# Kernel optimization log

Measured on AMD Instinct MI355X. Metric: run time of the kernel, lower is better.

The kernel has to match this reference:

```python
import jax, jax.numpy as jnp
import numpy as np
from jax import lax

L, B, N, D = 6, 4, 2048, 512
H, DH = 8, 64
ID = H * DH           # 512
M = 266               # int(64*log(64)) random features
INNER = 2 * D         # conformer expansion
K = 31                # depthwise kernel
PAD = (15, 15)        # calc_same_padding(31)
EPS_LN = 1e-5


def setup_inputs() -> dict:
    key = jax.random.key(0)
    ks = jax.random.split(key, 12)
    s = 0.02
    return {
        "x": jax.random.normal(ks[0], (B, N, D), jnp.float32),
        "ln1_g": jnp.ones((L, D), jnp.float32),
        "ln1_b": jnp.zeros((L, D), jnp.float32),
        "wq": jax.random.normal(ks[1], (L, ID, D), jnp.float32) * s,
        "bq": jnp.zeros((L, ID), jnp.float32),
        "wk": jax.random.normal(ks[2], (L, ID, D), jnp.float32) * s,
        "bk": jnp.zeros((L, ID), jnp.float32),
        "wv": jax.random.normal(ks[3], (L, ID, D), jnp.float32) * s,
        "bv": jnp.zeros((L, ID), jnp.float32),
        "wo": jax.random.normal(ks[4], (L, ID, D), jnp.float32) * s,
        "bo": jnp.zeros((L, D), jnp.float32),
        # FAVOR+ random projection buffer (gaussian orthogonal ~ iid gaussian rows)
        "proj": jax.random.normal(ks[5], (L, M, DH), jnp.float32),
        "ln2_g": jnp.ones((L, D), jnp.float32),
        "ln2_b": jnp.zeros((L, D), jnp.float32),
        "pw1_w": jax.random.normal(ks[6], (L, 2 * INNER, D), jnp.float32) * s,
        "pw1_b": jnp.zeros((L, 2 * INNER), jnp.float32),
        "dw_w": jax.random.normal(ks[7], (L, INNER, K), jnp.float32) * s,
        "dw_b": jnp.zeros((L, INNER), jnp.float32),
        "pw2_w": jax.random.normal(ks[8], (L, D, INNER), jnp.float32) * s,
        "pw2_b": jnp.zeros((L, D), jnp.float32),
    }


def layer_norm(x, g, b):
    mu = jnp.mean(x, axis=-1, keepdims=True)
    var = jnp.mean((x - mu) ** 2, axis=-1, keepdims=True)
    return (x - mu) * lax.rsqrt(var + EPS_LN) * g + b


def softmax_kernel(data, proj, is_query, eps=1e-4):
    # data: [b,h,n,dh], proj: [m,dh]
    dn = DH ** -0.25
    ratio = M ** -0.5
    data_dash = jnp.einsum('bhnd,md->bhnm', dn * data, proj)
    diag = jnp.sum(data * data, axis=-1, keepdims=True) * 0.5 * dn * dn  # [b,h,n,1]
    if is_query:
        mx = jnp.max(data_dash, axis=-1, keepdims=True)
        return ratio * (jnp.exp(data_dash - diag - mx) + eps)
    else:
        return ratio * jnp.exp(data_dash - diag + eps)


def favor_attention(q, k, v, proj):
    qp = softmax_kernel(q, proj, True)   # [b,h,n,m]
    kp = softmax_kernel(k, proj, False)  # [b,h,n,m]
    k_cumsum = jnp.sum(kp, axis=-2)      # [b,h,m]
    d_inv = 1.0 / (jnp.einsum('bhnm,bhm->bhn', qp, k_cumsum) + 1e-8)
    context = jnp.einsum('bhnm,bhne->bhme', kp, v)          # [b,h,m,dh]
    out = jnp.einsum('bhme,bhnm,bhn->bhne', context, qp, d_inv)
    return out


def pcmer_forward(x, ln1_g, ln1_b, wq, bq, wk, bk, wv, bv, wo, bo, proj,
                  ln2_g, ln2_b, pw1_w, pw1_b, dw_w, dw_b, pw2_w, pw2_b):
    for l in range(L):
        # --- self attention (FAVOR+) ---
        h = layer_norm(x, ln1_g[l], ln1_b[l])
        q = (h @ wq[l].T + bq[l]).reshape(B, N, H, DH).transpose(0, 2, 1, 3)
        k = (h @ wk[l].T + bk[l]).reshape(B, N, H, DH).transpose(0, 2, 1, 3)
        v = (h @ wv[l].T + bv[l]).reshape(B, N, H, DH).transpose(0, 2, 1, 3)
        o = favor_attention(q, k, v, proj[l])                 # [b,h,n,dh]
        o = o.transpose(0, 2, 1, 3).reshape(B, N, ID)
        x = x + (o @ wo[l].T + bo[l])
        # --- conformer conv module ---
        h = layer_norm(x, ln2_g[l], ln2_b[l])
        y = h @ pw1_w[l].T + pw1_b[l]                         # [b,n,2*inner]
        a, g = y[..., :INNER], y[..., INNER:]
        y = a * jax.nn.sigmoid(g)                             # GLU
        yt = jnp.pad(y.transpose(0, 2, 1), ((0, 0), (0, 0), PAD))  # [b,inner,n+30]
        dw = lax.conv_general_dilated(
            yt, dw_w[l][:, None, :], window_strides=(1,), padding='VALID',
            feature_group_count=INNER,
            dimension_numbers=('NCH', 'OIH', 'NCH')) + dw_b[l][None, :, None]
        dw = jax.nn.silu(dw).transpose(0, 2, 1)               # [b,n,inner]
        x = x + (dw @ pw2_w[l].T + pw2_b[l])
    return x


def reference(x, ln1_g, ln1_b, wq, bq, wk, bk, wv, bv, wo, bo, proj,
              ln2_g, ln2_b, pw1_w, pw1_b, dw_w, dw_b, pw2_w, pw2_b):
    return pcmer_forward(x, ln1_g, ln1_b, wq, bq, wk, bk, wv, bv, wo, bo, proj,
                         ln2_g, ln2_b, pw1_w, pw1_b, dw_w, dw_b, pw2_w, pw2_b)
```

## Files before the change

### kernel.cpp

```cpp
#include <hip/hip_runtime.h>


#define L_LAYERS 6
#define B_ 4
#define N_ 2048
#define D_ 512
#define H_ 8
#define DH_ 64
#define M_ 266
#define INNER_ 1024
#define T_ 8192
#define PS_ 320
#define QKVS_ 1536
#define NS_ 8

typedef __attribute__((ext_vector_type(8))) short short8;
typedef __attribute__((ext_vector_type(4))) float floatx4;

__device__ __forceinline__ ushort f2bf(float f) {
  union { float f; uint u; } v; v.f = f;
  uint r = v.u + 0x7fffu + ((v.u >> 16) & 1u);
  return (ushort)(r >> 16);
}
__device__ __forceinline__ float bf2f(ushort u) {
  union { uint u; float f; } v; v.u = ((uint)u) << 16;
  return v.f;
}
__device__ __forceinline__ float wave_sum(float v) {
#pragma unroll
  for (int m = 1; m < 64; m <<= 1) v += __shfl_xor(v, m);
  return v;
}
__device__ __forceinline__ void async_cp16(const void* g, void* l) {
  __builtin_amdgcn_global_load_lds(
      (const __attribute__((address_space(1))) void*)g,
      (__attribute__((address_space(3))) void*)l, 16, 0, 0);
}

__global__ void f2bf4_dual(const float4* __restrict__ s1, int n1,
                           const float4* __restrict__ s2, int n2,
                           ushort* __restrict__ out) {
  int i = blockIdx.x * 256 + threadIdx.x;
  if (i >= n1 + n2) return;
  float4 v = (i < n1) ? s1[i] : s2[i - n1];
  ushort4 r;
  r.x = f2bf(v.x); r.y = f2bf(v.y); r.z = f2bf(v.z); r.w = f2bf(v.w);
  *(ushort4*)(out + (size_t)i * 4) = r;
}
__global__ void pack_qkv_w3(const float4* __restrict__ wq, const float4* __restrict__ wk,
                            const float4* __restrict__ wv, ushort* __restrict__ dst) {
  int i = blockIdx.x * 256 + threadIdx.x;
  const int per = L_LAYERS * 512 * 128;
  if (i >= 3 * per) return;
  int seg = i / per;
  int rem = i - seg * per;
  const float4* src = seg == 0 ? wq : (seg == 1 ? wk : wv);
  int l = rem >> 16;
  int r2 = rem & 65535;
  int row = r2 >> 7, c4 = r2 & 127;
  float4 v = src[rem];
  ushort4 r;
  r.x = f2bf(v.x); r.y = f2bf(v.y); r.z = f2bf(v.z); r.w = f2bf(v.w);
  *(ushort4*)(dst + ((size_t)l * QKVS_ + seg * 512 + row) * 512 + c4 * 4) = r;
}
__global__ void pack_small(const float* __restrict__ bq, const float* __restrict__ bk,
                           const float* __restrict__ bv, float* __restrict__ bqkv,
                           const float* __restrict__ proj, ushort* __restrict__ pjp,
                           const float* __restrict__ pw1b, float* __restrict__ pb1) {
  int i = blockIdx.x * 256 + threadIdx.x;
  const int A = L_LAYERS * QKVS_;
  const int Bn = L_LAYERS * 320 * 64;
  const int C = L_LAYERS * 2048;
  if (i < A) {
    int l = i / QKVS_, c = i % QKVS_;
    bqkv[i] = c < 512 ? bq[l * 512 + c]
                      : (c < 1024 ? bk[l * 512 + c - 512] : bv[l * 512 + c - 1024]);
  } else if (i < A + Bn) {
    int j = i - A;
    int l = j / (320 * 64), rem = j % (320 * 64), m = rem >> 6, kk = rem & 63;
    pjp[j] = (m < M_) ? f2bf(proj[((size_t)l * M_ + m) * 64 + kk]) : (ushort)0;
  } else if (i < A + Bn + C) {
    int j = i - A - Bn;
    int l = j >> 11, cp = j & 2047;
    int s = (cp >> 4) & 1;
    int srow = ((cp >> 5) << 4) + (cp & 15) + s * 1024;
    pb1[j] = pw1b[l * 2048 + srow];
  }
}
__global__ void pack_pw1_w(const float4* __restrict__ src, ushort* __restrict__ dst) {
  int i = blockIdx.x * 256 + threadIdx.x;
  if (i >= L_LAYERS * 2048 * 128) return;
  int l = i >> 18;
  int rem = i & 262143;
  int cp = rem >> 7, c4 = rem & 127;
  int s = (cp >> 4) & 1;
  int srow = ((cp >> 5) << 4) + (cp & 15) + s * 1024;
  float4 v = src[((size_t)l * 2048 + srow) * 128 + c4];
  ushort4 r;
  r.x = f2bf(v.x); r.y = f2bf(v.y); r.z = f2bf(v.z); r.w = f2bf(v.w);
  *(ushort4*)(dst + ((size_t)l * 2048 + cp) * 512 + c4 * 4) = r;
}

__global__ __launch_bounds__(256) void ln_kernel(const float* __restrict__ x,
                                                 const float* __restrict__ g,
                                                 const float* __restrict__ b,
                                                 ushort* __restrict__ out) {
  const int t = blockIdx.x;
  const int tid = threadIdx.x;
  const float* row = x + (size_t)t * D_;
  float v0 = row[tid], v1 = row[tid + 256];
  float s1 = v0 + v1;
  float s2 = v0 * v0 + v1 * v1;
  s1 = wave_sum(s1);
  s2 = wave_sum(s2);
  __shared__ float sh1[4], sh2[4];
  int w = tid >> 6;
  if ((tid & 63) == 0) { sh1[w] = s1; sh2[w] = s2; }
  __syncthreads();
  s1 = sh1[0] + sh1[1] + sh1[2] + sh1[3];
  s2 = sh2[0] + sh2[1] + sh2[2] + sh2[3];
  float mu = s1 * (1.f / D_);
  float var = s2 * (1.f / D_) - mu * mu;
  float rs = rsqrtf(var + 1e-5f);
  out[(size_t)t * D_ + tid]       = f2bf((v0 - mu) * rs * g[tid] + b[tid]);
  out[(size_t)t * D_ + tid + 256] = f2bf((v1 - mu) * rs * g[tid + 256] + b[tid + 256]);
}

template <bool HAS_RES, bool OUT_BF16, int ACT, int KT, int BUFS>
__global__ __launch_bounds__(256) void gemm_mfma(const ushort* __restrict__ A,
                                                 const ushort* __restrict__ W,
                                                 const float* __restrict__ bias,
                                                 const float* __restrict__ res,
                                                 void* __restrict__ Cout,
                                                 int ldc) {
  constexpr int NT = KT / 32;
  __shared__ ushort As[BUFS][128 * 32];
  __shared__ ushort Bs[BUFS][128 * 32];
  const int tid = threadIdx.x;
  const int w = tid >> 6, lane = tid & 63;
  const int row0 = blockIdx.x * 128, col0 = blockIdx.y * 128;
  const int rl = lane >> 2;
  const int lc = ((lane & 3) ^ ((lane >> 3) & 3)) * 8;
  const ushort* gA0 = A + (size_t)(row0 + w * 32 + rl) * KT + lc;
  const ushort* gA1 = gA0 + (size_t)16 * KT;
  const ushort* gB0 = W + (size_t)(col0 + w * 32 + rl) * KT + lc;
  const ushort* gB1 = gB0 + (size_t)16 * KT;
  const int m16 = lane & 15, quad = lane >> 4;
  const int awr = (w >> 1) * 64, bwc = (w & 1) * 64;
  floatx4 acc[4][4] = {};

  auto stage = [&](int t, int buf) {
    async_cp16(gA0 + t * 32, As[buf] + w * 1024);
    async_cp16(gA1 + t * 32, As[buf] + w * 1024 + 512);
    async_cp16(gB0 + t * 32, Bs[buf] + w * 1024);
    async_cp16(gB1 + t * 32, Bs[buf] + w * 1024 + 512);
  };
  auto body = [&](int buf, bool bar2) {
    short8 af[4], bfr[4];
#pragma unroll
    for (int i = 0; i < 4; i++) {
      int r = awr + i * 16 + m16;
      af[i] = *(const short8*)&As[buf][r * 32 + (quad ^ ((r >> 1) & 3)) * 8];
    }
#pragma unroll
    for (int j = 0; j < 4; j++) {
      int r = bwc + j * 16 + m16;
      bfr[j] = *(const short8*)&Bs[buf][r * 32 + (quad ^ ((r >> 1) & 3)) * 8];
    }
    if (bar2) {
      asm volatile("s_waitcnt lgkmcnt(0)" ::: "memory");
      __builtin_amdgcn_sched_barrier(0);
      __builtin_amdgcn_s_barrier();
    }
#pragma unroll
    for (int i = 0; i < 4; i++)
#pragma unroll
      for (int j = 0; j < 4; j++)
        acc[i][j] = __builtin_amdgcn_mfma_f32_16x16x32_bf16(af[i], bfr[j], acc[i][j], 0, 0, 0);
  };

  stage(0, 0);
  if (BUFS == 3) stage(1, 1);
  int c = 0;
  for (int t = 0; t < NT - (BUFS - 1); t++) {
    int pf = c + (BUFS - 1); if (pf >= BUFS) pf -= BUFS;
    stage(t + BUFS - 1, pf);
    if (BUFS == 3) { asm volatile("s_waitcnt vmcnt(8)" ::: "memory"); }
    else           { asm volatile("s_waitcnt vmcnt(4)" ::: "memory"); }
    __builtin_amdgcn_s_barrier();
    body(c, true);
    c++; if (c >= BUFS) c -= BUFS;
  }
  if (BUFS == 3) {
    asm volatile("s_waitcnt vmcnt(4)" ::: "memory");
    __builtin_amdgcn_s_barrier();
    body(c, false);
    c++; if (c >= BUFS) c -= BUFS;
  }
  asm volatile("s_waitcnt vmcnt(0)" ::: "memory");
  __builtin_amdgcn_s_barrier();
  body(c, false);

  if (ACT == 0) {
#pragma unroll
    for (int i = 0; i < 4; i++) {
      const int r0 = row0 + awr + i * 16 + quad * 4;
#pragma unroll
      for (int j = 0; j < 4; j++) {
        const int cc = col0 + bwc + j * 16 + m16;
        const float bv = bias[cc];
#pragma unroll
        for (int r = 0; r < 4; r++) {
          float vv = acc[i][j][r] + bv;
          if (HAS_RES) vv += res[(size_t)(r0 + r) * ldc + cc];
          if (OUT_BF16) ((ushort*)Cout)[(size_t)(r0 + r) * ldc + cc] = f2bf(vv);
          else          ((float*)Cout)[(size_t)(r0 + r) * ldc + cc] = vv;
        }
      }
    }
  } else {
#pragma unroll
    for (int i = 0; i < 4; i++) {
      const int r0 = row0 + awr + i * 16 + quad * 4;
#pragma unroll
      for (int jp = 0; jp < 2; jp++) {
        const int j = jp * 2;
        const int ca = col0 + bwc + j * 16 + m16;
        const float ba = bias[ca], bg = bias[ca + 16];
        const int oc = ((col0 + bwc) >> 1) + jp * 16 + m16;
#pragma unroll
        for (int r = 0; r < 4; r++) {
          float a = acc[i][j][r] + ba;
          float g = acc[i][j + 1][r] + bg;
          float z = a / (1.f + __expf(-g));
          ((ushort*)Cout)[(size_t)(r0 + r) * ldc + oc] = f2bf(z);
        }
      }
    }
  }
}

__global__ __launch_bounds__(256) void ctx_phi_mfma(const ushort* __restrict__ qkv,
                                                    const ushort* __restrict__ projp,
                                                    float* __restrict__ part,
                                                    float* __restrict__ kpart) {
  __shared__ ushort projs[64 * 64];
  __shared__ ushort kts[32 * 64];
  __shared__ ushort kps[64][40];
  __shared__ ushort vsT[64][40];
  __shared__ float diag_sh[32];
  __shared__ float kshare[4][64];
  const int bh = blockIdx.x, mt = blockIdx.y, ns = blockIdx.z;
  const int b = bh >> 3, h = bh & 7;
  const int m0 = mt * 64;
  const int tid = threadIdx.x;
  const int w = tid >> 6, lane = tid & 63, l16 = lane & 15, quad = lane >> 4;
  const int rl8 = lane >> 3;
  const int lc8 = ((lane & 7) ^ (rl8 & 7)) * 8;
#pragma unroll
  for (int j = 0; j < 2; j++) {
    const int rb = w * 16 + j * 8;
    async_cp16(projp + (size_t)(m0 + rb + rl8) * 64 + lc8, projs + rb * 64);
  }
  const int nn = tid >> 3;
  const int a8 = tid & 7;
  const int gn = nn >> 3, jn = nn & 7;
  const int pc = ((gn ^ (a8 & 3)) << 3) | jn;
  const int km = tid & 63, kg = tid >> 6;
  const float dn = 0.35355339059327373f;
  const float ratio = 0.06131393394849658f;
  floatx4 acc[4] = {};
  float ksp = 0.f;
  for (int nstep = 0; nstep < 2048 / NS_ / 32; nstep++) {
    const int n0 = ns * (2048 / NS_) + nstep * 32;
    {
      const int rb = w * 8;
      async_cp16(qkv + (size_t)(b * N_ + n0 + rb + rl8) * QKVS_ + 512 + h * 64 + lc8,
                 kts + rb * 64);
    }
    uint4 vv = *(const uint4*)(qkv + ((size_t)(b * N_ + n0 + nn)) * QKVS_ + 1024 + h * 64 + a8 * 8);
    __syncthreads();
    {
      const int r = tid >> 3;
      const int c = tid & 7;
      short8 kv8 = *(const short8*)&kts[r * 64 + c * 8];
      const ushort* u = (const ushort*)&kv8;
      float s = 0.f;
#pragma unroll
      for (int j = 0; j < 8; j++) { float f = bf2f(u[j]); s += f * f; }
      s += __shfl_xor(s, 1);
      s += __shfl_xor(s, 2);
      s += __shfl_xor(s, 4);
      if ((tid & 7) == 0) diag_sh[r] = 0.0625f * s;
    }
    {
      const ushort* ve = (const ushort*)&vv;
#pragma unroll
      for (int j = 0; j < 8; j++) vsT[a8 * 8 + j][pc] = ve[j];
    }
    __syncthreads();
    floatx4 pacc[2] = {};
    __builtin_amdgcn_s_setprio(1);
#pragma unroll
    for (int s = 0; s < 2; s++) {
      const int ar = w * 16 + l16;
      short8 af = *(const short8*)&projs[ar * 64 + ((s * 4 + quad) ^ (ar & 7)) * 8];
#pragma unroll
      for (int nj = 0; nj < 2; nj++) {
        const int br = nj * 16 + l16;
        short8 bf = *(const short8*)&kts[br * 64 + ((s * 4 + quad) ^ (br & 7)) * 8];
        pacc[nj] = __builtin_amdgcn_mfma_f32_16x16x32_bf16(af, bf, pacc[nj], 0, 0, 0);
      }
    }
    __builtin_amdgcn_s_setprio(0);
#pragma unroll
    for (int nj = 0; nj < 2; nj++) {
      const int n = nj * 16 + l16;
      const float dgn = diag_sh[n];
#pragma unroll
      for (int r = 0; r < 4; r++) {
        const int m = w * 16 + quad * 4 + r;
        float val = (m0 + m < M_) ? ratio * __expf(dn * pacc[nj][r] - dgn + 1e-4f) : 0.f;
        kps[m][(((n >> 3) ^ ((m >> 3) & 3)) << 3) | (n & 7)] = f2bf(val);
      }
    }
    __syncthreads();
    const int am = w * 16 + l16;
    const int apg = quad ^ ((am >> 3) & 3);
    short8 af = *(const short8*)&kps[am][apg * 8];
    __builtin_amdgcn_s_setprio(1);
#pragma unroll
    for (int et = 0; et < 4; et++) {
      const int be = et * 16 + l16;
      const int bpg = quad ^ ((be >> 3) & 3);
      short8 bf = *(const short8*)&vsT[be][bpg * 8];
      acc[et] = __builtin_amdgcn_mfma_f32_16x16x32_bf16(af, bf, acc[et], 0, 0, 0);
    }
    __builtin_amdgcn_s_setprio(0);
    {
      short8 kr = *(const short8*)&kps[km][kg * 8];
      const ushort* ku = (const ushort*)&kr;
#pragma unroll
      for (int j = 0; j < 8; j++) ksp += bf2f(ku[j]);
    }
  }
  float* pb = part + ((size_t)(bh * NS_ + ns) * 5 + mt) * 4096;
#pragma unroll
  for (int et = 0; et < 4; et++)
#pragma unroll
    for (int r = 0; r < 4; r++)
      pb[(w * 16 + quad * 4 + r) * 64 + et * 16 + l16] = acc[et][r];
  kshare[kg][km] = ksp;
  __syncthreads();
  if (tid < 64)
    kpart[((size_t)(bh * NS_ + ns) * 5 + mt) * 64 + tid] =
        kshare[0][tid] + kshare[1][tid] + kshare[2][tid] + kshare[3][tid];
}

__global__ __launch_bounds__(256) void ctx_reduce(const float* __restrict__ part,
                                                  const float* __restrict__ kpart,
                                                  ushort* __restrict__ ctxbT,
                                                  float* __restrict__ ksum) {
  const int bh = blockIdx.x, mt = blockIdx.y;
  const int tid = threadIdx.x;
  const int w = tid >> 6, lane = tid & 63;
  for (int oc = w; oc < 8; oc += 4) {
    const int mbase = mt * 64 + oc * 8;
    if (mbase < 288) {
      float s[8] = {0.f, 0.f, 0.f, 0.f, 0.f, 0.f, 0.f, 0.f};
#pragma unroll
      for (int ns = 0; ns < NS_; ns++) {
        const float* pb = part + ((size_t)(bh * NS_ + ns) * 5 + mt) * 4096;
#pragma unroll
        for (int ml = 0; ml < 8; ml++) s[ml] += pb[(oc * 8 + ml) * 64 + lane];
      }
      ushort tmp[8];
#pragma unroll
      for (int ml = 0; ml < 8; ml++) tmp[ml] = f2bf(s[ml]);
      *(short8*)(ctxbT + ((size_t)(bh * 64 + lane)) * 288 + mbase) = *(const short8*)tmp;
    }
  }
  if (tid < 64) {
    float s = 0.f;
#pragma unroll
    for (int ns = 0; ns < NS_; ns++)
      s += kpart[((size_t)(bh * NS_ + ns) * 5 + mt) * 64 + tid];
    ksum[(size_t)bh * PS_ + mt * 64 + tid] = s;
  }
}

__global__ __launch_bounds__(256, 4) void attn_fused(const ushort* __restrict__ qkv,
                                                     const ushort* __restrict__ projp,
                                                     const ushort* __restrict__ ctxbT,
                                                     const float* __restrict__ ksum,
                                                     ushort* __restrict__ o) {
  __shared__ __align__(16) ushort Bs[160 * 64];
  __shared__ __align__(16) ushort qst[64][40];
  __shared__ __align__(16) ushort outs[64][64];
  __shared__ float ks_sh[288];
  const int bh = blockIdx.x, b = bh >> 3, h = bh & 7;
  const int n0 = blockIdx.y * 64;
  const int tid = threadIdx.x;
  const int w = tid >> 6, lane = tid & 63, l16 = lane & 15, quad = lane >> 4;
  const int rl8 = lane >> 3;
  const int lc8 = ((lane & 7) ^ (rl8 & 7)) * 8;
#pragma unroll
  for (int j = 0; j < 5; j++) {
    const int rb = w * 40 + j * 8;
    async_cp16(projp + (size_t)(rb + rl8) * 64 + lc8, Bs + rb * 64);
  }
  for (int i = tid; i < 288; i += 256) ks_sh[i] = ksum[(size_t)bh * PS_ + i];
  const ushort* qrow = qkv + (size_t)(b * N_ + n0 + w * 16 + l16) * QKVS_ + h * 64;
  short8 q0 = *(const short8*)(qrow + quad * 8);
  short8 q1 = *(const short8*)(qrow + 32 + quad * 8);
  float dv = 0.f;
  {
    const ushort* u0 = (const ushort*)&q0;
    const ushort* u1 = (const ushort*)&q1;
#pragma unroll
    for (int j = 0; j < 8; j++) {
      float f0 = bf2f(u0[j]), f1 = bf2f(u1[j]);
      dv += f0 * f0 + f1 * f1;
    }
  }
  dv += __shfl_xor(dv, 16);
  dv += __shfl_xor(dv, 32);
  dv *= 0.0625f;
  float dgr[4];
#pragma unroll
  for (int r = 0; r < 4; r++) dgr[r] = __shfl(dv, quad * 4 + r, 16);
  __syncthreads();
  floatx4 acc[18];
#pragma unroll
  for (int cf = 0; cf < 18; cf++) acc[cf] = (floatx4){0.f, 0.f, 0.f, 0.f};
  __builtin_amdgcn_s_setprio(1);
#pragma unroll
  for (int s = 0; s < 2; s++) {
    short8 af = s ? q1 : q0;
#pragma unroll
    for (int cf = 0; cf < 10; cf++) {
      const int br = cf * 16 + l16;
      short8 bf = *(const short8*)&Bs[br * 64 + ((s * 4 + quad) ^ (br & 7)) * 8];
      acc[cf] = __builtin_amdgcn_mfma_f32_16x16x32_bf16(af, bf, acc[cf], 0, 0, 0);
    }
  }
  __builtin_amdgcn_s_setprio(0);
  __syncthreads();
#pragma unroll
  for (int j = 0; j < 4; j++) {
    const int rb = w * 32 + j * 8;
    async_cp16(projp + (size_t)(160 + rb + rl8) * 64 + lc8, Bs + rb * 64);
  }
  __syncthreads();
  __builtin_amdgcn_s_setprio(1);
#pragma unroll
  for (int s = 0; s < 2; s++) {
    short8 af = s ? q1 : q0;
#pragma unroll
    for (int cf = 10; cf < 18; cf++) {
      const int br = (cf - 10) * 16 + l16;
      short8 bf = *(const short8*)&Bs[br * 64 + ((s * 4 + quad) ^ (br & 7)) * 8];
      acc[cf] = __builtin_amdgcn_mfma_f32_16x16x32_bf16(af, bf, acc[cf], 0, 0, 0);
    }
  }
  __builtin_amdgcn_s_setprio(0);
  const float dn = 0.35355339059327373f;
  const float ratio = 0.06131393394849658f;
  float mxr[4];
#pragma unroll
  for (int r = 0; r < 4; r++) {
    float v[18];
#pragma unroll
    for (int cf = 0; cf < 18; cf++) {
      const int col = cf * 16 + l16;
      v[cf] = (col < M_) ? dn * acc[cf][r] : -1e30f;
    }
#pragma unroll
    for (int st = 1; st < 18; st <<= 1)
#pragma unroll
      for (int k = 0; k + st < 18; k += 2 * st) v[k] = fmaxf(v[k], v[k + st]);
    float mx = v[0];
    mx = fmaxf(mx, __shfl_xor(mx, 1));
    mx = fmaxf(mx, __shfl_xor(mx, 2));
    mx = fmaxf(mx, __shfl_xor(mx, 4));
    mx = fmaxf(mx, __shfl_xor(mx, 8));
    mxr[r] = mx;
  }
  float dacc[4] = {0.f, 0.f, 0.f, 0.f};
  floatx4 acc2[4] = {};
  const ushort* ctxrow = ctxbT + (size_t)bh * (64 * 288);
  for (int m0 = 0; m0 < 288; m0 += 32) {
    const int cf0 = m0 >> 4;
#pragma unroll
    for (int cc = 0; cc < 2; cc++) {
      const int col = m0 + cc * 16 + l16;
      const float kv = ks_sh[col];
#pragma unroll
      for (int r = 0; r < 4; r++) {
        float val = (col < M_) ? ratio * (__expf(dn * acc[cf0 + cc][r] - dgr[r] - mxr[r]) + 1e-4f)
                               : 0.f;
        qst[w * 16 + quad * 4 + r][cc * 16 + l16] = f2bf(val);
        dacc[r] += val * kv;
      }
    }
    short8 af = *(const short8*)&qst[w * 16 + l16][quad * 8];
    __builtin_amdgcn_s_setprio(1);
#pragma unroll
    for (int et = 0; et < 4; et++) {
      short8 bf = *(const short8*)(ctxrow + (size_t)(et * 16 + l16) * 288 + m0 + quad * 8);
      acc2[et] = __builtin_amdgcn_mfma_f32_16x16x32_bf16(af, bf, acc2[et], 0, 0, 0);
    }
    __builtin_amdgcn_s_setprio(0);
  }
  float di[4];
#pragma unroll
  for (int r = 0; r < 4; r++) {
    float d = dacc[r];
    d += __shfl_xor(d, 1);
    d += __shfl_xor(d, 2);
    d += __shfl_xor(d, 4);
    d += __shfl_xor(d, 8);
    di[r] = 1.f / (d + 1e-8f);
  }
#pragma unroll
  for (int r = 0; r < 4; r++)
#pragma unroll
    for (int et = 0; et < 4; et++)
      outs[w * 16 + quad * 4 + r][et * 16 + l16] = f2bf(acc2[et][r] * di[r]);
#pragma unroll
  for (int j = 0; j < 2; j++) {
    const int lr = j * 8 + (lane >> 3);
    short8 ov = *(const short8*)&outs[w * 16 + lr][(lane & 7) * 8];
    *(short8*)(o + (size_t)(b * N_ + n0 + w * 16 + lr) * 512 + h * 64 + (lane & 7) * 8) = ov;
  }
}

#define TN_ 32
__global__ __launch_bounds__(256) void dwconv_kernel(const ushort* __restrict__ x,
                                                     const float* __restrict__ w,
                                                     const float* __restrict__ bias,
                                                     ushort* __restrict__ out) {
  const int bid = blockIdx.x;
  const int cb = bid & 3;
  const int nb = (bid >> 2) & (N_ / TN_ - 1);
  const int b  = bid >> 8;
  const int c = cb * 256 + threadIdx.x;
  const int n0 = nb * TN_;
  float win[TN_ + 30];
#pragma unroll
  for (int i = 0; i < TN_ + 30; i++) {
    int nn = n0 + i - 15;
    win[i] = (nn >= 0 && nn < N_) ? bf2f(x[(size_t)(b * N_ + nn) * INNER_ + c]) : 0.f;
  }
  float wc[31];
#pragma unroll
  for (int kk = 0; kk < 31; kk++) wc[kk] = w[c * 31 + kk];
  const float bsv = bias[c];
#pragma unroll
  for (int j = 0; j < TN_; j++) {
    float acc = bsv;
#pragma unroll
    for (int kk = 0; kk < 31; kk++) acc += win[j + kk] * wc[kk];
    acc = acc / (1.f + __expf(-acc));
    out[(size_t)(b * N_ + n0 + j) * INNER_ + c] = f2bf(acc);
  }
}

extern "C" void kernel_launch(void* const* d_in, const int* in_sizes, int n_in,
                              void* d_out, int out_size, void* d_ws, size_t ws_size,
                              hipStream_t stream) {
  const float* in_x  = (const float*)d_in[0];
  const float* ln1_g = (const float*)d_in[1];
  const float* ln1_b = (const float*)d_in[2];
  const float* wq    = (const float*)d_in[3];
  const float* bq    = (const float*)d_in[4];
  const float* wk    = (const float*)d_in[5];
  const float* bk    = (const float*)d_in[6];
  const float* wv    = (const float*)d_in[7];
  const float* bv    = (const float*)d_in[8];
  const float* wo    = (const float*)d_in[9];
  const float* bo    = (const float*)d_in[10];
  const float* proj  = (const float*)d_in[11];
  const float* ln2_g = (const float*)d_in[12];
  const float* ln2_b = (const float*)d_in[13];
  const float* pw1_w = (const float*)d_in[14];
  const float* pw1_b = (const float*)d_in[15];
  const float* dw_w  = (const float*)d_in[16];
  const float* dw_b  = (const float*)d_in[17];
  const float* pw2_w = (const float*)d_in[18];
  const float* pw2_b = (const float*)d_in[19];

  char* cur = (char*)d_ws;
  auto alloc = [&](size_t bytes) { char* p = cur; cur += (bytes + 255) & ~(size_t)255; return p; };
  float*  x    = (float*)alloc((size_t)T_ * D_ * 4);
  ushort* p    = (ushort*)alloc((size_t)T_ * INNER_ * 2 * 2);
  float*  part = (float*)alloc((size_t)32 * NS_ * 5 * 4096 * 4);
  float*  kpart= (float*)alloc((size_t)32 * NS_ * 5 * 64 * 4);
  ushort* ctxb = (ushort*)alloc((size_t)32 * 288 * 64 * 2);
  float*  ksum = (float*)alloc((size_t)32 * PS_ * 4);
  ushort* h    = (ushort*)alloc((size_t)T_ * D_ * 2);
  ushort* qkv  = (ushort*)alloc((size_t)T_ * QKVS_ * 2);
  ushort* obuf = (ushort*)alloc((size_t)T_ * D_ * 2);
  ushort* wqkv_b = (ushort*)alloc((size_t)L_LAYERS * QKVS_ * 512 * 2);
  float*  bqkv   = (float*)alloc((size_t)L_LAYERS * QKVS_ * 4);
  ushort* wo_b = (ushort*)alloc((size_t)L_LAYERS * D_ * D_ * 2 + (size_t)L_LAYERS * D_ * INNER_ * 2);
  ushort* p2_b = wo_b + (size_t)L_LAYERS * D_ * D_;
  ushort* pjp  = (ushort*)alloc((size_t)L_LAYERS * 320 * 64 * 2);
  ushort* p1_b = (ushort*)alloc((size_t)L_LAYERS * 2048 * D_ * 2);
  float*  pb1  = (float*)alloc((size_t)L_LAYERS * 2048 * 4);
  ushort* glu  = p;
  ushort* conv = p + (size_t)T_ * INNER_;

  pack_qkv_w3<<<(3 * L_LAYERS * 512 * 128 + 255) / 256, 256, 0, stream>>>(
      (const float4*)wq, (const float4*)wk, (const float4*)wv, wqkv_b);
  pack_pw1_w<<<(L_LAYERS * 2048 * 128 + 255) / 256, 256, 0, stream>>>((const float4*)pw1_w, p1_b);
  {
    int n1 = L_LAYERS * D_ * D_ / 4;
    int n2 = L_LAYERS * D_ * INNER_ / 4;
    f2bf4_dual<<<(n1 + n2 + 255) / 256, 256, 0, stream>>>(
        (const float4*)wo, n1, (const float4*)pw2_w, n2, wo_b);
  }
  {
    int tot = L_LAYERS * QKVS_ + L_LAYERS * 320 * 64 + L_LAYERS * 2048;
    pack_small<<<(tot + 255) / 256, 256, 0, stream>>>(bq, bk, bv, bqkv, proj, pjp, pw1_b, pb1);
  }

  for (int l = 0; l < L_LAYERS; l++) {
    const ushort* wqkvl = wqkv_b + (size_t)l * QKVS_ * 512;
    const ushort* wol = wo_b + (size_t)l * D_ * D_;
    const ushort* pjl = pjp + (size_t)l * 320 * 64;
    const ushort* p1l = p1_b + (size_t)l * 2048 * D_;
    const ushort* p2l = p2_b + (size_t)l * D_ * INNER_;
    const float*  dwl = dw_w + (size_t)l * INNER_ * 31;
    const float*  dwbl = dw_b + (size_t)l * INNER_;
    const float*  xin = (l == 0) ? in_x : x;
    float* xout = (l == L_LAYERS - 1) ? (float*)d_out : x;

    ln_kernel<<<T_, 256, 0, stream>>>(xin, ln1_g + l * D_, ln1_b + l * D_, h);
    gemm_mfma<false, true, 0, 512, 3><<<dim3(T_ / 128, QKVS_ / 128), 256, 0, stream>>>(
        h, wqkvl, bqkv + (size_t)l * QKVS_, nullptr, qkv, QKVS_);
    ctx_phi_mfma<<<dim3(32, 5, NS_), 256, 0, stream>>>(qkv, pjl, part, kpart);
    ctx_reduce<<<dim3(32, 5), 256, 0, stream>>>(part, kpart, ctxb, ksum);
    attn_fused<<<dim3(32, 32), 256, 0, stream>>>(qkv, pjl, ctxb, ksum, obuf);
    gemm_mfma<true, false, 0, 512, 3><<<dim3(T_ / 128, 4), 256, 0, stream>>>(
        obuf, wol, bo + l * D_, xin, x, D_);
    ln_kernel<<<T_, 256, 0, stream>>>(x, ln2_g + l * D_, ln2_b + l * D_, h);
    gemm_mfma<false, true, 1, 512, 2><<<dim3(T_ / 128, 16), 256, 0, stream>>>(
        h, p1l, pb1 + (size_t)l * 2048, nullptr, glu, INNER_);
    dwconv_kernel<<<B_ * (N_ / TN_) * 4, 256, 0, stream>>>(glu, dwl, dwbl, conv);
    gemm_mfma<true, false, 0, 1024, 3><<<dim3(T_ / 128, 4), 256, 0, stream>>>(
        conv, p2l, pw2_b + l * D_, x, xout, D_);
  }
}
```

Baseline: 1.177 ms.

## Wave-per-row layernorm, double-buffer K tiles in ctx_phi, prefetch ctx in attention

LayerNorm now gives each wavefront one row, using float4 loads and a single 16-byte bf16 store. This removes the shared-memory reduction and the block barrier, and the launch grid shrinks by four. ctx_phi_mfma double-buffers the K tile through async copies with explicit vmcnt waits and raw s_barrier, so the next tile's load overlaps the current compute. attn_fused prefetches the next ctx B-fragments into registers ahead of the MFMAs. The hand-written waitcnt counts are fragile and the extra registers may lower occupancy.

```diff
diff --git a/kernel.cpp b/kernel.cpp
--- a/kernel.cpp
+++ b/kernel.cpp
@@ -105,25 +105,26 @@
                                                  const float* __restrict__ g,
                                                  const float* __restrict__ b,
                                                  ushort* __restrict__ out) {
-  const int t = blockIdx.x;
-  const int tid = threadIdx.x;
-  const float* row = x + (size_t)t * D_;
-  float v0 = row[tid], v1 = row[tid + 256];
-  float s1 = v0 + v1;
-  float s2 = v0 * v0 + v1 * v1;
+  const int w = threadIdx.x >> 6, lane = threadIdx.x & 63;
+  const int t = blockIdx.x * 4 + w;
+  const float4* row = (const float4*)(x + (size_t)t * D_);
+  float4 v0 = row[lane * 2];
+  float4 v1 = row[lane * 2 + 1];
+  float s1 = v0.x + v0.y + v0.z + v0.w + v1.x + v1.y + v1.z + v1.w;
+  float s2 = v0.x * v0.x + v0.y * v0.y + v0.z * v0.z + v0.w * v0.w +
+             v1.x * v1.x + v1.y * v1.y + v1.z * v1.z + v1.w * v1.w;
   s1 = wave_sum(s1);
   s2 = wave_sum(s2);
-  __shared__ float sh1[4], sh2[4];
-  int w = tid >> 6;
-  if ((tid & 63) == 0) { sh1[w] = s1; sh2[w] = s2; }
-  __syncthreads();
-  s1 = sh1[0] + sh1[1] + sh1[2] + sh1[3];
-  s2 = sh2[0] + sh2[1] + sh2[2] + sh2[3];
   float mu = s1 * (1.f / D_);
   float var = s2 * (1.f / D_) - mu * mu;
   float rs = rsqrtf(var + 1e-5f);
-  out[(size_t)t * D_ + tid]       = f2bf((v0 - mu) * rs * g[tid] + b[tid]);
-  out[(size_t)t * D_ + tid + 256] = f2bf((v1 - mu) * rs * g[tid + 256] + b[tid + 256]);
+  const int c0 = lane * 8;
+  float vv[8] = {v0.x, v0.y, v0.z, v0.w, v1.x, v1.y, v1.z, v1.w};
+  ushort o8[8];
+#pragma unroll
+  for (int j = 0; j < 8; j++)
+    o8[j] = f2bf((vv[j] - mu) * rs * g[c0 + j] + b[c0 + j]);
+  *(short8*)(out + (size_t)t * D_ + c0) = *(const short8*)o8;
 }
 
 template <bool HAS_RES, bool OUT_BF16, int ACT, int KT, int BUFS>
@@ -245,7 +246,7 @@
                                                     float* __restrict__ part,
                                                     float* __restrict__ kpart) {
   __shared__ ushort projs[64 * 64];
-  __shared__ ushort kts[32 * 64];
+  __shared__ ushort kts[2][32 * 64];
   __shared__ ushort kps[64][40];
   __shared__ ushort vsT[64][40];
   __shared__ float diag_sh[32];
@@ -257,10 +258,17 @@
   const int w = tid >> 6, lane = tid & 63, l16 = lane & 15, quad = lane >> 4;
   const int rl8 = lane >> 3;
   const int lc8 = ((lane & 7) ^ (rl8 & 7)) * 8;
+  constexpr int NT = 2048 / NS_ / 32;
+  const int nbase = ns * (2048 / NS_);
 #pragma unroll
   for (int j = 0; j < 2; j++) {
     const int rb = w * 16 + j * 8;
     async_cp16(projp + (size_t)(m0 + rb + rl8) * 64 + lc8, projs + rb * 64);
+  }
+  {
+    const int rb = w * 8;
+    async_cp16(qkv + (size_t)(b * N_ + nbase + rb + rl8) * QKVS_ + 512 + h * 64 + lc8,
+               kts[0] + rb * 64);
   }
   const int nn = tid >> 3;
   const int a8 = tid & 7;
@@ -271,19 +279,23 @@
   const float ratio = 0.06131393394849658f;
   floatx4 acc[4] = {};
   float ksp = 0.f;
-  for (int nstep = 0; nstep < 2048 / NS_ / 32; nstep++) {
-    const int n0 = ns * (2048 / NS_) + nstep * 32;
-    {
+#pragma unroll
+  for (int t = 0; t < NT; t++) {
+    const int n0 = nbase + t * 32;
+    const int cur = t & 1;
+    uint4 vv = *(const uint4*)(qkv + ((size_t)(b * N_ + n0 + nn)) * QKVS_ + 1024 + h * 64 + a8 * 8);
+    if (t + 1 < NT) {
       const int rb = w * 8;
-      async_cp16(qkv + (size_t)(b * N_ + n0 + rb + rl8) * QKVS_ + 512 + h * 64 + lc8,
-                 kts + rb * 64);
-    }
-    uint4 vv = *(const uint4*)(qkv + ((size_t)(b * N_ + n0 + nn)) * QKVS_ + 1024 + h * 64 + a8 * 8);
-    __syncthreads();
+      async_cp16(qkv + (size_t)(b * N_ + n0 + 32 + rb + rl8) * QKVS_ + 512 + h * 64 + lc8,
+                 kts[cur ^ 1] + rb * 64);
+    }
+    if (t + 1 < NT) { asm volatile("s_waitcnt vmcnt(2)" ::: "memory"); }
+    else            { asm volatile("s_waitcnt vmcnt(1)" ::: "memory"); }
+    __builtin_amdgcn_s_barrier();
     {
       const int r = tid >> 3;
       const int c = tid & 7;
-      short8 kv8 = *(const short8*)&kts[r * 64 + c * 8];
+      short8 kv8 = *(const short8*)&kts[cur][r * 64 + c * 8];
       const ushort* u = (const ushort*)&kv8;
       float s = 0.f;
 #pragma unroll
@@ -298,7 +310,9 @@
 #pragma unroll
       for (int j = 0; j < 8; j++) vsT[a8 * 8 + j][pc] = ve[j];
     }
-    __syncthreads();
+    asm volatile("s_waitcnt lgkmcnt(0)" ::: "memory");
+    __builtin_amdgcn_sched_barrier(0);
+    __builtin_amdgcn_s_barrier();
     floatx4 pacc[2] = {};
     __builtin_amdgcn_s_setprio(1);
 #pragma unroll
@@ -308,7 +322,7 @@
 #pragma unroll
       for (int nj = 0; nj < 2; nj++) {
         const int br = nj * 16 + l16;
-        short8 bf = *(const short8*)&kts[br * 64 + ((s * 4 + quad) ^ (br & 7)) * 8];
+        short8 bf = *(const short8*)&kts[cur][br * 64 + ((s * 4 + quad) ^ (br & 7)) * 8];
         pacc[nj] = __builtin_amdgcn_mfma_f32_16x16x32_bf16(af, bf, pacc[nj], 0, 0, 0);
       }
     }
@@ -324,7 +338,9 @@
         kps[m][(((n >> 3) ^ ((m >> 3) & 3)) << 3) | (n & 7)] = f2bf(val);
       }
     }
-    __syncthreads();
+    asm volatile("s_waitcnt lgkmcnt(0)" ::: "memory");
+    __builtin_amdgcn_sched_barrier(0);
+    __builtin_amdgcn_s_barrier();
     const int am = w * 16 + l16;
     const int apg = quad ^ ((am >> 3) & 3);
     short8 af = *(const short8*)&kps[am][apg * 8];
@@ -489,6 +505,11 @@
   float dacc[4] = {0.f, 0.f, 0.f, 0.f};
   floatx4 acc2[4] = {};
   const ushort* ctxrow = ctxbT + (size_t)bh * (64 * 288);
+  short8 bfc[4];
+#pragma unroll
+  for (int et = 0; et < 4; et++)
+    bfc[et] = *(const short8*)(ctxrow + (size_t)(et * 16 + l16) * 288 + quad * 8);
+#pragma unroll
   for (int m0 = 0; m0 < 288; m0 += 32) {
     const int cf0 = m0 >> 4;
 #pragma unroll
@@ -503,14 +524,22 @@
         dacc[r] += val * kv;
       }
     }
+    short8 bfn[4];
+    if (m0 + 32 < 288) {
+#pragma unroll
+      for (int et = 0; et < 4; et++)
+        bfn[et] = *(const short8*)(ctxrow + (size_t)(et * 16 + l16) * 288 + m0 + 32 + quad * 8);
+    }
     short8 af = *(const short8*)&qst[w * 16 + l16][quad * 8];
     __builtin_amdgcn_s_setprio(1);
 #pragma unroll
-    for (int et = 0; et < 4; et++) {
-      short8 bf = *(const short8*)(ctxrow + (size_t)(et * 16 + l16) * 288 + m0 + quad * 8);
-      acc2[et] = __builtin_amdgcn_mfma_f32_16x16x32_bf16(af, bf, acc2[et], 0, 0, 0);
-    }
+    for (int et = 0; et < 4; et++)
+      acc2[et] = __builtin_amdgcn_mfma_f32_16x16x32_bf16(af, bfc[et], acc2[et], 0, 0, 0);
     __builtin_amdgcn_s_setprio(0);
+    if (m0 + 32 < 288) {
+#pragma unroll
+      for (int et = 0; et < 4; et++) bfc[et] = bfn[et];
+    }
   }
   float di[4];
 #pragma unroll
@@ -636,7 +665,7 @@
     const float*  xin = (l == 0) ? in_x : x;
     float* xout = (l == L_LAYERS - 1) ? (float*)d_out : x;
 
-    ln_kernel<<<T_, 256, 0, stream>>>(xin, ln1_g + l * D_, ln1_b + l * D_, h);
+    ln_kernel<<<T_ / 4, 256, 0, stream>>>(xin, ln1_g + l * D_, ln1_b + l * D_, h);
     gemm_mfma<false, true, 0, 512, 3><<<dim3(T_ / 128, QKVS_ / 128), 256, 0, stream>>>(
         h, wqkvl, bqkv + (size_t)l * QKVS_, nullptr, qkv, QKVS_);
     ctx_phi_mfma<<<dim3(32, 5, NS_), 256, 0, stream>>>(qkv, pjl, part, kpart);
@@ -644,7 +673,7 @@
     attn_fused<<<dim3(32, 32), 256, 0, stream>>>(qkv, pjl, ctxb, ksum, obuf);
     gemm_mfma<true, false, 0, 512, 3><<<dim3(T_ / 128, 4), 256, 0, stream>>>(
         obuf, wol, bo + l * D_, xin, x, D_);
-    ln_kernel<<<T_, 256, 0, stream>>>(x, ln2_g + l * D_, ln2_b + l * D_, h);
+    ln_kernel<<<T_ / 4, 256, 0, stream>>>(x, ln2_g + l * D_, ln2_b + l * D_, h);
     gemm_mfma<false, true, 1, 512, 2><<<dim3(T_ / 128, 16), 256, 0, stream>>>(
         h, p1l, pb1 + (size_t)l * 2048, nullptr, glu, INNER_);
     dwconv_kernel<<<B_ * (N_ / TN_) * 4, 256, 0, stream>>>(glu, dwl, dwbl, conv);
```

Measured after the change: 1.377 ms. 17.0% more time.
